# Kernel optimization log

Measured on AMD Instinct MI355X. Metric: run time of the kernel, lower is better.

The kernel has to match this reference:

```python
import jax, jax.numpy as jnp
import numpy as np

INSIZE = 512
OUTSIZE = 512
N_U = 64
N_V = 64
SIGMA_MIN = 0.1
SIGMA_MAX = 1.0
BATCH = 8192


def setup_inputs() -> dict:
    key = jax.random.key(0)
    kx, kp, ku, kv, kb = jax.random.split(key, 5)
    x = jax.random.normal(kx, (BATCH, INSIZE), dtype=jnp.float32)
    nsigma = min(INSIZE, OUTSIZE)
    p = 0.001 * jax.random.normal(kp, (nsigma,), dtype=jnp.float32)
    U = jnp.triu(jax.random.normal(ku, (INSIZE, INSIZE), dtype=jnp.float32))
    V = jnp.triu(jax.random.normal(kv, (OUTSIZE, OUTSIZE), dtype=jnp.float32))
    bound = 1.0 / float(np.sqrt(INSIZE))
    bias = jax.random.uniform(kb, (1, OUTSIZE), minval=-bound, maxval=bound, dtype=jnp.float32)
    return {"x": x, "p": p, "U": U, "V": V, "bias": bias}


def _house_chain(x, rows):
    # Sequentially apply Householder reflections. rows[i] has its leading
    # entries zeroed (upper-triangular structure), which makes the full-width
    # dot/outer-product exactly equal to torch's Hprod on the trailing slice
    # u[-k:] while leaving the leading columns of x untouched.
    def step(x, u):
        alpha = 2.0 * (x @ u) / jnp.dot(u, u)  # [B]
        return x - alpha[:, None] * u[None, :], None
    x, _ = jax.lax.scan(step, x, rows)
    return x


def _sigma_matrix(p, dtype):
    r = (SIGMA_MAX - SIGMA_MIN) / 2.0
    sigma_mean = SIGMA_MIN + r
    sigmas = 2.0 * r * (jax.nn.sigmoid(p) - 0.5) + sigma_mean  # [nsigma]
    nsigma = min(INSIZE, OUTSIZE)
    idx = jnp.arange(nsigma)
    return jnp.zeros((INSIZE, OUTSIZE), dtype=dtype).at[idx, idx].set(sigmas.astype(dtype))


def reference(x, p, U, V, bias):
    # Umultiply: i = 0 .. N_U-1, reflector U[i] with k = insize - i
    x = _house_chain(x, jnp.triu(U)[:N_U])
    # x @ Sigma (rectangular diagonal of constrained singular values)
    x = x @ _sigma_matrix(p, x.dtype)
    # Vmultiply: i = N_V-1 down to 0, reflector V[i] with k = outsize - i
    x = _house_chain(x, jnp.triu(V)[:N_V][::-1])
    return x + bias
```

## Files before the change

kernel.cpp:

```cpp
#include <hip/hip_runtime.h>
#include <hip/hip_bf16.h>
#include <math.h>


#define INSIZE 512
#define NREF 64
#define BATCH 8192

static constexpr int OFF_WT    = 0;
static constexpr int OFF_SIGMA = 131072;
static constexpr int OFF_BETAU = OFF_SIGMA + 512;
static constexpr int OFF_BETAV = OFF_BETAU + 64;
static constexpr int OFF_GU    = OFF_BETAV + 64;
static constexpr int OFF_GV    = OFF_GU + 4096;
static constexpr int OFF_C     = OFF_GV + 4096;
static constexpr int OFF_PT    = OFF_C + 4096;
static constexpr int OFF_R     = OFF_PT + 128 * 512;

__device__ inline float sigma_of(float pv) {
    float s = 1.0f / (1.0f + expf(-pv));
    return 0.55f + 0.9f * (s - 0.5f);
}

__global__ __launch_bounds__(256) void k_prep(const float* __restrict__ U,
                                              const float* __restrict__ V,
                                              const float* __restrict__ p,
                                              float* __restrict__ ws) {
    int b = blockIdx.x, t = threadIdx.x;
    if (b == 192) {
        for (int c = t; c < INSIZE; c += 256)
            (ws + OFF_SIGMA)[c] = sigma_of(p[c]);
        return;
    }
    __shared__ float rowi[INSIZE];
    int w = t >> 6, l = t & 63;
    if (b < 128) {
        bool isV = (b >= 64);
        int i = isV ? (b - 64) : b;
        const float* src = isV ? V : U;
        int srow = isV ? (63 - i) : i;
        for (int c = t; c < INSIZE; c += 256) rowi[c] = src[srow * INSIZE + c];
        __syncthreads();
        float* G = ws + (isV ? OFF_GV : OFF_GU);
        float* beta = ws + (isV ? OFF_BETAV : OFF_BETAU);
        for (int jj = 0; jj < 16; ++jj) {
            int j = w * 16 + jj;
            int jrow = isV ? (63 - j) : j;
            const float* rj = src + jrow * INSIZE;
            float s = 0.f;
            for (int c = l; c < INSIZE; c += 64) s += rowi[c] * rj[c];
            for (int o = 32; o > 0; o >>= 1) s += __shfl_down(s, o, 64);
            if (l == 0) {
                G[i * 64 + j] = s;
                if (j == i) beta[i] = 2.0f / s;
            }
        }
    } else {
        int i = b - 128;
        for (int c = t; c < INSIZE; c += 256)
            rowi[c] = U[i * INSIZE + c] * sigma_of(p[c]);
        __syncthreads();
        float* C = ws + OFF_C;
        for (int jj = 0; jj < 16; ++jj) {
            int j = w * 16 + jj;
            const float* rj = V + (63 - j) * INSIZE;
            float s = 0.f;
            for (int c = l; c < INSIZE; c += 64) s += rowi[c] * rj[c];
            for (int o = 32; o > 0; o >>= 1) s += __shfl_down(s, o, 64);
            if (l == 0) C[i * 64 + j] = s;
        }
    }
}

__global__ __launch_bounds__(512) void k_AR(const float* __restrict__ U,
                                            const float* __restrict__ V,
                                            float* __restrict__ ws) {
    __shared__ float Gs[64 * 64];
    __shared__ float bs[64];
    int z = blockIdx.x;
    int t = threadIdx.x;
    const float* G = ws + (z ? OFF_GV : OFF_GU);
    const float* beta = ws + (z ? OFF_BETAV : OFF_BETAU);
    for (int i = t; i < 1024; i += 512)
        *(float4*)&Gs[i * 4] = *(const float4*)&G[i * 4];
    if (t < 64) bs[t] = beta[t];
    __syncthreads();
    float part[64];
    if (z == 0) {
        float* At = ws + OFF_PT;
#pragma unroll
        for (int j = 0; j < 64; ++j) part[j] = U[j * INSIZE + t];
#pragma unroll
        for (int m = 0; m < 64; ++m) {
            float am = part[m] * bs[m];
            part[m] = am;
#pragma unroll
            for (int j = m + 1; j < 64; ++j)
                part[j] -= am * Gs[m * 64 + j];
        }
#pragma unroll
        for (int j = 0; j < 64; ++j) At[j * INSIZE + t] = part[j];
    } else {
        float* R = ws + OFF_R;
#pragma unroll
        for (int i = 0; i < 64; ++i) part[i] = V[(63 - i) * INSIZE + t];
#pragma unroll
        for (int i = 63; i >= 0; --i) {
            float s = part[i];
#pragma unroll
            for (int m = i + 1; m < 64; ++m)
                s -= Gs[i * 64 + m] * part[m];
            part[i] = s * bs[i];
        }
#pragma unroll
        for (int i = 0; i < 64; ++i) R[i * INSIZE + t] = part[i];
    }
}

__global__ __launch_bounds__(256) void k_WtE(const float* __restrict__ U,
                                             const float* __restrict__ V,
                                             float* __restrict__ ws) {
    __shared__ float Ps[128][34];
    __shared__ float Qs[128][34];
    __shared__ float Cs[4096];
    int t = threadIdx.x;
    int r0 = (blockIdx.x >> 4) * 32;
    int c0 = (blockIdx.x & 15) * 32;
    const float* At = ws + OFF_PT;
    const float* R = ws + OFF_R;
    const float* sig = ws + OFF_SIGMA;
    int lr = t & 31, kb = t >> 5;
    float sc = sig[c0 + lr];
#pragma unroll
    for (int ii = 0; ii < 8; ++ii) {
        int k = kb + ii * 8;
        Ps[k][lr] = At[k * INSIZE + r0 + lr];
    }
#pragma unroll
    for (int ii = 0; ii < 16; ++ii) {
        int k = kb + ii * 8;
        Qs[k][lr] = (k < 64) ? U[k * INSIZE + c0 + lr] * sc
                             : R[(k - 64) * INSIZE + c0 + lr];
    }
#pragma unroll
    for (int i = 0; i < 16; ++i) Cs[t + i * 256] = (ws + OFF_C)[t + i * 256];
    __syncthreads();
    float sr = sig[r0 + lr];
#pragma unroll
    for (int ii = 0; ii < 8; ++ii) {
        int j = kb * 8 + ii;
        float e = sr * V[(63 - j) * INSIZE + r0 + lr];
#pragma unroll 8
        for (int i = 0; i < 64; ++i)
            e -= Ps[i][lr] * Cs[i * 64 + j];
        Ps[64 + j][lr] = e;
    }
    __syncthreads();
    int ty = t >> 4, tx = t & 15;
    float a00 = 0.f, a01 = 0.f, a10 = 0.f, a11 = 0.f;
#pragma unroll
    for (int k = 0; k < 128; ++k) {
        float2 a = *(const float2*)&Ps[k][ty * 2];
        float2 bq = *(const float2*)&Qs[k][tx * 2];
        a00 += a.x * bq.x; a01 += a.x * bq.y;
        a10 += a.y * bq.x; a11 += a.y * bq.y;
    }
    int rg = r0 + ty * 2, cg = c0 + tx * 2;
    float w00 = ((rg == cg) ? sig[rg] : 0.f) - a00;
    float w01 = ((rg == cg + 1) ? sig[rg] : 0.f) - a01;
    float w10 = ((rg + 1 == cg) ? sig[rg + 1] : 0.f) - a10;
    float w11 = ((rg + 1 == cg + 1) ? sig[rg + 1] : 0.f) - a11;
    unsigned short* Wt = (unsigned short*)(ws + OFF_WT);
    __hip_bfloat162 lo = __float22bfloat162_rn(make_float2(w00, w10));
    __hip_bfloat162 hi = __float22bfloat162_rn(make_float2(w01, w11));
    *(__hip_bfloat162*)&Wt[cg * INSIZE + rg] = lo;
    *(__hip_bfloat162*)&Wt[(cg + 1) * INSIZE + rg] = hi;
}

typedef __attribute__((ext_vector_type(8))) short short8;
typedef __attribute__((ext_vector_type(4))) float float4v;

__global__ __launch_bounds__(256) void k_gemm(const float* __restrict__ X,
                                              const float* __restrict__ ws,
                                              const float* __restrict__ bias,
                                              float* __restrict__ out) {
    __shared__ float As[64 * 32];
    __shared__ unsigned short Bs[128 * 32];
    const unsigned short* Wt = (const unsigned short*)(ws + OFF_WT);

    int L = blockIdx.x;
    int inner = L & 7;
    int bn = (L >> 3) & 3;
    int bm = (L >> 5) * 8 + inner;
    int row0 = bm * 64, col0 = bn * 128;

    int t = threadIdx.x;
    int l = t & 63, w = t >> 6;
    int wm = (w & 1) * 32, wn = (w >> 1) * 64;

    float4v acc[2][4] = {};
    int quad = l >> 4;
    int lan = l & 15;

    for (int k0 = 0; k0 < INSIZE; k0 += 32) {
        __syncthreads();
#pragma unroll
        for (int i = 0; i < 2; ++i) {
            int P = i * 256 + t;
            int prow = P >> 3, pc = P & 7;
            int lc = pc ^ (prow & 7);
            const float* g = X + (size_t)(row0 + prow) * INSIZE + k0 + lc * 4;
            __builtin_amdgcn_global_load_lds(
                (const __attribute__((address_space(1))) void*)g,
                (__attribute__((address_space(3))) void*)(As + P * 4), 16, 0, 0);
        }
#pragma unroll
        for (int i = 0; i < 2; ++i) {
            int P = i * 256 + t;
            int prow = P >> 2, pc = P & 3;
            int lc = pc ^ ((prow >> 1) & 3);
            const unsigned short* g = Wt + (size_t)(col0 + prow) * INSIZE + k0 + lc * 8;
            __builtin_amdgcn_global_load_lds(
                (const __attribute__((address_space(1))) void*)g,
                (__attribute__((address_space(3))) void*)(Bs + P * 8), 16, 0, 0);
        }
        __syncthreads();

        short8 af[2];
        short8 bf[4];
#pragma unroll
        for (int mi = 0; mi < 2; ++mi) {
            int rl = wm + mi * 16 + lan;
            int c0q = quad * 2;
            const float4v lo = *(const float4v*)(As + (rl * 8 + (c0q ^ (rl & 7))) * 4);
            const float4v hi = *(const float4v*)(As + (rl * 8 + ((c0q + 1) ^ (rl & 7))) * 4);
            union { short8 s; __hip_bfloat162 h[4]; } u;
            u.h[0] = __float22bfloat162_rn(make_float2(lo[0], lo[1]));
            u.h[1] = __float22bfloat162_rn(make_float2(lo[2], lo[3]));
            u.h[2] = __float22bfloat162_rn(make_float2(hi[0], hi[1]));
            u.h[3] = __float22bfloat162_rn(make_float2(hi[2], hi[3]));
            af[mi] = u.s;
        }
#pragma unroll
        for (int ni = 0; ni < 4; ++ni) {
            int rn = wn + ni * 16 + lan;
            int c = quad ^ ((rn >> 1) & 3);
            bf[ni] = *(const short8*)(Bs + (rn * 4 + c) * 8);
        }
#pragma unroll
        for (int mi = 0; mi < 2; ++mi)
#pragma unroll
            for (int ni = 0; ni < 4; ++ni)
                acc[mi][ni] = __builtin_amdgcn_mfma_f32_16x16x32_bf16(
                    af[mi], bf[ni], acc[mi][ni], 0, 0, 0);
    }

#pragma unroll
    for (int ni = 0; ni < 4; ++ni) {
        int c = col0 + wn + ni * 16 + lan;
        float bv = bias[c];
#pragma unroll
        for (int mi = 0; mi < 2; ++mi) {
            int rbase = row0 + wm + mi * 16 + quad * 4;
#pragma unroll
            for (int r = 0; r < 4; ++r)
                out[(size_t)(rbase + r) * INSIZE + c] = acc[mi][ni][r] + bv;
        }
    }
}

extern "C" void kernel_launch(void* const* d_in, const int* in_sizes, int n_in,
                              void* d_out, int out_size, void* d_ws, size_t ws_size,
                              hipStream_t stream) {
    const float* x    = (const float*)d_in[0];
    const float* p    = (const float*)d_in[1];
    const float* U    = (const float*)d_in[2];
    const float* V    = (const float*)d_in[3];
    const float* bias = (const float*)d_in[4];
    float* ws  = (float*)d_ws;
    float* out = (float*)d_out;

    k_prep<<<193, 256, 0, stream>>>(U, V, p, ws);
    k_AR<<<2, 512, 0, stream>>>(U, V, ws);
    k_WtE<<<256, 256, 0, stream>>>(U, V, ws);
    k_gemm<<<512, 256, 0, stream>>>(x, ws, bias, out);
}
```

Baseline: 125.5 us.

## Fuse triangular solve kernel into WtE, recomputing per-tile slices redundantly

Drops the separate 2-block k_AR kernel that performed the 64-step triangular recurrences for U and V over all 512 columns. Each k_WtE block now computes only the 32 columns it needs, using one wave for the U side and one for the V side, and keeps the results in shared memory. This removes a kernel launch and a low-parallelism serial stage, plus its round trip of intermediates through global memory. The cost is redundant recomputation across blocks and only 64 of 256 threads being busy during that phase.

After: 131.8 us. +5.1%, slower.

```diff
diff --git a/kernel.cpp b/kernel.cpp
--- a/kernel.cpp
+++ b/kernel.cpp
@@ -14,8 +14,6 @@
 static constexpr int OFF_GU    = OFF_BETAV + 64;
 static constexpr int OFF_GV    = OFF_GU + 4096;
 static constexpr int OFF_C     = OFF_GV + 4096;
-static constexpr int OFF_PT    = OFF_C + 4096;
-static constexpr int OFF_R     = OFF_PT + 128 * 512;
 
 __device__ inline float sigma_of(float pv) {
     float s = 1.0f / (1.0f + expf(-pv));
@@ -72,79 +70,74 @@
     }
 }
 
-__global__ __launch_bounds__(512) void k_AR(const float* __restrict__ U,
-                                            const float* __restrict__ V,
-                                            float* __restrict__ ws) {
-    __shared__ float Gs[64 * 64];
-    __shared__ float bs[64];
-    int z = blockIdx.x;
-    int t = threadIdx.x;
-    const float* G = ws + (z ? OFF_GV : OFF_GU);
-    const float* beta = ws + (z ? OFF_BETAV : OFF_BETAU);
-    for (int i = t; i < 1024; i += 512)
-        *(float4*)&Gs[i * 4] = *(const float4*)&G[i * 4];
-    if (t < 64) bs[t] = beta[t];
-    __syncthreads();
-    float part[64];
-    if (z == 0) {
-        float* At = ws + OFF_PT;
-#pragma unroll
-        for (int j = 0; j < 64; ++j) part[j] = U[j * INSIZE + t];
-#pragma unroll
-        for (int m = 0; m < 64; ++m) {
-            float am = part[m] * bs[m];
-            part[m] = am;
-#pragma unroll
-            for (int j = m + 1; j < 64; ++j)
-                part[j] -= am * Gs[m * 64 + j];
-        }
-#pragma unroll
-        for (int j = 0; j < 64; ++j) At[j * INSIZE + t] = part[j];
-    } else {
-        float* R = ws + OFF_R;
-#pragma unroll
-        for (int i = 0; i < 64; ++i) part[i] = V[(63 - i) * INSIZE + t];
-#pragma unroll
-        for (int i = 63; i >= 0; --i) {
-            float s = part[i];
-#pragma unroll
-            for (int m = i + 1; m < 64; ++m)
-                s -= Gs[i * 64 + m] * part[m];
-            part[i] = s * bs[i];
-        }
-#pragma unroll
-        for (int i = 0; i < 64; ++i) R[i * INSIZE + t] = part[i];
-    }
-}
-
 __global__ __launch_bounds__(256) void k_WtE(const float* __restrict__ U,
                                              const float* __restrict__ V,
                                              float* __restrict__ ws) {
     __shared__ float Ps[128][34];
     __shared__ float Qs[128][34];
-    __shared__ float Cs[4096];
+    __shared__ float Xs[4160];
     int t = threadIdx.x;
     int r0 = (blockIdx.x >> 4) * 32;
     int c0 = (blockIdx.x & 15) * 32;
-    const float* At = ws + OFF_PT;
-    const float* R = ws + OFF_R;
     const float* sig = ws + OFF_SIGMA;
+    float* Qf = &Qs[0][0];
+
+    for (int i = t; i < 1024; i += 256) {
+        *(float4*)&Xs[i * 4] = *(const float4*)&(ws + OFF_GU)[i * 4];
+        *(float4*)&Qf[i * 4] = *(const float4*)&(ws + OFF_GV)[i * 4];
+    }
+    if (t < 64) {
+        Xs[4096 + t] = (ws + OFF_BETAU)[t];
+        Qf[4096 + t] = (ws + OFF_BETAV)[t];
+    }
+    __syncthreads();
+
+    float partR[64];
+    if (t < 32) {
+        int r = r0 + t;
+        float part[64];
+#pragma unroll
+        for (int j = 0; j < 64; ++j) part[j] = U[j * INSIZE + r];
+#pragma unroll
+        for (int m = 0; m < 64; ++m) {
+            float am = part[m] * Xs[4096 + m];
+            part[m] = am;
+#pragma unroll
+            for (int j = m + 1; j < 64; ++j)
+                part[j] -= am * Xs[m * 64 + j];
+        }
+#pragma unroll
+        for (int j = 0; j < 64; ++j) Ps[j][t] = part[j];
+    } else if (t < 64) {
+        int c = c0 + (t - 32);
+#pragma unroll
+        for (int i = 0; i < 64; ++i) partR[i] = V[(63 - i) * INSIZE + c];
+#pragma unroll
+        for (int i = 63; i >= 0; --i) {
+            float s = partR[i];
+#pragma unroll
+            for (int m = i + 1; m < 64; ++m)
+                s -= Qf[i * 64 + m] * partR[m];
+            partR[i] = s * Qf[4096 + i];
+        }
+    }
+    __syncthreads();
+
+    for (int i = t; i < 1024; i += 256)
+        *(float4*)&Xs[i * 4] = *(const float4*)&(ws + OFF_C)[i * 4];
     int lr = t & 31, kb = t >> 5;
     float sc = sig[c0 + lr];
 #pragma unroll
     for (int ii = 0; ii < 8; ++ii) {
         int k = kb + ii * 8;
-        Ps[k][lr] = At[k * INSIZE + r0 + lr];
-    }
-#pragma unroll
-    for (int ii = 0; ii < 16; ++ii) {
-        int k = kb + ii * 8;
-        Qs[k][lr] = (k < 64) ? U[k * INSIZE + c0 + lr] * sc
-                             : R[(k - 64) * INSIZE + c0 + lr];
-    }
-#pragma unroll
-    for (int i = 0; i < 16; ++i) Cs[t + i * 256] = (ws + OFF_C)[t + i * 256];
-    __syncthreads();
+        Qs[k][lr] = U[k * INSIZE + c0 + lr] * sc;
+    }
+    if (t >= 32 && t < 64) {
+#pragma unroll
+        for (int i = 0; i < 64; ++i) Qs[64 + i][t - 32] = partR[i];
+    }
+    __syncthreads();
+
     float sr = sig[r0 + lr];
 #pragma unroll
     for (int ii = 0; ii < 8; ++ii) {
@@ -152,10 +145,11 @@
         float e = sr * V[(63 - j) * INSIZE + r0 + lr];
 #pragma unroll 8
         for (int i = 0; i < 64; ++i)
-            e -= Ps[i][lr] * Cs[i * 64 + j];
+            e -= Ps[i][lr] * Xs[i * 64 + j];
         Ps[64 + j][lr] = e;
     }
     __syncthreads();
+
     int ty = t >> 4, tx = t & 15;
     float a00 = 0.f, a01 = 0.f, a10 = 0.f, a11 = 0.f;
 #pragma unroll
@@ -281,7 +275,6 @@
     float* out = (float*)d_out;
 
     k_prep<<<193, 256, 0, stream>>>(U, V, p, ws);
-    k_AR<<<2, 512, 0, stream>>>(U, V, ws);
     k_WtE<<<256, 256, 0, stream>>>(U, V, ws);
     k_gemm<<<512, 256, 0, stream>>>(x, ws, bias, out);
 }
```
